# Kernel optimization log

Hardware: AMD Instinct MI355X
Metric: run time of the kernel (lower is better)

The kernel has to match this reference:

```python
import jax, jax.numpy as jnp
import numpy as np

NEG = -1e30  # stand-in for -inf that keeps logaddexp grad-safe


def _ctc_neg_log_likelihood(predictions, labels):
    # predictions: [B, T, C] logits; labels: [B, L] int, -1 = padding.
    # tf.nn.ctc_loss(blank_index=-1) => blank class is C-1.
    B, T, C = predictions.shape
    L = labels.shape[1]
    S = 2 * L + 1
    blank = C - 1

    label_len = jnp.sum((labels != -1).astype(jnp.int32), axis=-1)  # [B]
    labels_c = jnp.where(labels < 0, 0, labels).astype(jnp.int32)

    # Extended label sequence: blank, l1, blank, l2, ..., blank  -> [B, S]
    ext = jnp.full((B, S), blank, dtype=jnp.int32)
    ext = ext.at[:, 1::2].set(labels_c)

    # s-2 transition allowed only at label positions (odd s) with ext[s] != ext[s-2]
    same = jnp.concatenate([jnp.zeros((B, 2), bool), ext[:, 2:] == ext[:, :-2]], axis=1)
    is_label_pos = (jnp.arange(S) % 2 == 1)[None, :]
    allow2 = is_label_pos & ~same  # [B, S]

    # valid extended positions per example: s < 2*label_len + 1
    valid = jnp.arange(S)[None, :] < (2 * label_len + 1)[:, None]  # [B, S]

    log_probs = jax.nn.log_softmax(predictions, axis=-1)  # [B, T, C]
    # emission log-prob for each extended-label slot: [B, T, S]
    lp_ext = jnp.take_along_axis(log_probs, jnp.broadcast_to(ext[:, None, :], (B, T, S)), axis=2)

    has_lab = label_len > 0
    alpha0 = jnp.full((B, S), NEG, dtype=log_probs.dtype)
    alpha0 = alpha0.at[:, 0].set(lp_ext[:, 0, 0])
    alpha0 = alpha0.at[:, 1].set(jnp.where(has_lab, lp_ext[:, 0, 1], NEG))
    alpha0 = jnp.where(valid, alpha0, NEG)

    def step(alpha, lp_t):
        a1 = alpha
        a2 = jnp.pad(alpha, ((0, 0), (1, 0)), constant_values=NEG)[:, :S]
        a3 = jnp.pad(alpha, ((0, 0), (2, 0)), constant_values=NEG)[:, :S]
        a3 = jnp.where(allow2, a3, NEG)
        new = jnp.logaddexp(jnp.logaddexp(a1, a2), a3) + lp_t
        new = jnp.where(valid, new, NEG)
        return new, None

    lp_rest = jnp.moveaxis(lp_ext[:, 1:], 1, 0)  # [T-1, B, S]
    alphaT, _ = jax.lax.scan(step, alpha0, lp_rest)

    idx1 = (2 * label_len)[:, None]              # final blank
    idx2 = jnp.maximum(idx1 - 1, 0)              # final label
    a_end1 = jnp.take_along_axis(alphaT, idx1, axis=1)[:, 0]
    a_end2 = jnp.take_along_axis(alphaT, idx2, axis=1)[:, 0]
    a_end2 = jnp.where(has_lab, a_end2, NEG)
    log_lik = jnp.logaddexp(a_end1, a_end2)
    return -log_lik  # [B]


def setup_inputs() -> dict:
    key = jax.random.key(0)
    k1, k2 = jax.random.split(key)
    B, T, C, L = 1024, 384, 96, 48
    labels = jax.random.randint(k1, (B, L), 0, C - 1).astype(jnp.int64)
    predictions = jax.random.normal(k2, (B, T, C), dtype=jnp.float32)
    return {"labels": labels, "predictions": predictions}


def reference(labels, predictions):
    per_example = _ctc_neg_log_likelihood(predictions, labels)
    return jnp.mean(per_example)
```

## Files before the change

kernel.cpp:

```cpp
#include <hip/hip_runtime.h>

#define NEG (-1e30f)

constexpr int Tt = 384;
constexpr int Cc = 96;
constexpr int Ll = 48;
constexpr int Gg = 8;
constexpr int NG = 24;

__device__ __forceinline__ float lae2(float a, float b) {
    float m = fmaxf(a, b);
    return m + __logf(__expf(a - m) + __expf(b - m));
}
__device__ __forceinline__ float lae3(float a, float b, float c) {
    float m = fmaxf(fmaxf(a, b), c);
    return m + __logf(__expf(a - m) + __expf(b - m) + __expf(c - m));
}

template <bool FWD>
__device__ __forceinline__ void half_pass(const float2* __restrict__ rp2, int lane,
                                          int idx_h, int bitsel, bool allow2,
                                          bool valid_e, bool valid_o,
                                          float& st_e, float& st_o) {
    float2 q[Gg];
    float lpbC[Gg], lplC[Gg], lpbN[Gg], lplN[Gg];

    auto loadg = [&](int g) {
#pragma unroll
        for (int j = 0; j < Gg; ++j) {
            int k = g * Gg + j;
            int t = FWD ? k : (Tt - 1 - k);
            q[j] = (lane < 48) ? rp2[(size_t)t * 48 + lane] : make_float2(NEG, NEG);
        }
    };
    auto lp_from_q = [&](float* lpb, float* lpl, int gnext) {
        float s[Gg], gb[Gg], g0[Gg], g1[Gg];
#pragma unroll
        for (int j = 0; j < Gg; ++j)
            s[j] = (lane < 48) ? (__expf(q[j].x) + __expf(q[j].y)) : 0.0f;
#pragma unroll
        for (int j = 0; j < Gg; ++j) {
            gb[j] = __shfl(q[j].y, 47, 64);
            g0[j] = __shfl(q[j].x, idx_h, 64);
            g1[j] = __shfl(q[j].y, idx_h, 64);
        }
        if (gnext < NG) loadg(gnext);
#pragma unroll
        for (int off = 32; off >= 1; off >>= 1) {
#pragma unroll
            for (int j = 0; j < Gg; ++j) s[j] += __shfl_xor(s[j], off, 64);
        }
#pragma unroll
        for (int j = 0; j < Gg; ++j) {
            float lz = __logf(s[j]);
            lpb[j] = gb[j] - lz;
            lpl[j] = (bitsel ? g1[j] : g0[j]) - lz;
        }
    };

    loadg(0);
    lp_from_q(lpbC, lplC, 1);

    for (int g = 0; g < NG; ++g) {
        if (g + 1 < NG) lp_from_q(lpbN, lplN, g + 2);
#pragma unroll
        for (int j = 0; j < Gg; ++j) {
            if (FWD) {
                float ap = __shfl_up(st_o, 1, 64);
                ap = lane ? ap : NEG;
                float ne = lae2(st_e, ap) + lpbC[j];
                float no = lae3(st_o, st_e, allow2 ? ap : NEG) + lplC[j];
                st_e = valid_e ? ne : NEG;
                st_o = valid_o ? no : NEG;
            } else {
                float en = __shfl_down(st_e, 1, 64);
                float on = __shfl_down(st_o, 1, 64);
                float ne = lae2(st_e, st_o) + lpbC[j];
                float no = lae3(st_o, en, allow2 ? on : NEG) + lplC[j];
                st_e = valid_e ? ne : NEG;
                st_o = valid_o ? no : NEG;
            }
        }
        if (g + 1 < NG) {
#pragma unroll
            for (int j = 0; j < Gg; ++j) { lpbC[j] = lpbN[j]; lplC[j] = lplN[j]; }
        }
    }
}

__global__ __launch_bounds__(64) void zero_kernel(float* o) { *o = 0.0f; }

__global__ __launch_bounds__(128) void ctc_fb(const int* __restrict__ labels,
                                              const float* __restrict__ pred,
                                              float* __restrict__ out,
                                              float invB) {
    const int b    = blockIdx.x;
    const int lane = threadIdx.x & 63;
    const int wv   = threadIdx.x >> 6;
    const float2* rp2 = (const float2*)(pred + (size_t)b * Tt * Cc);

    int v = (lane < Ll) ? labels[(size_t)b * Ll + lane] : -1;
    int present = (lane < Ll) && (v != -1);
    int labv = (v < 0) ? 0 : v;
    unsigned long long pm = __ballot(present);
    int len = __popcll(pm);

    bool valid_e = (lane <= len);
    bool valid_o = (lane < len);
    int idx_h  = labv >> 1;
    int bitsel = labv & 1;
    int lab_p = __shfl_up(labv, 1, 64);
    int lab_n = __shfl_down(labv, 1, 64);

    __shared__ float sbe[64], sbo[64];

    float A_e = NEG, A_o = NEG;
    if (wv == 0) {
        bool allow2 = (lane >= 1) && (labv != lab_p);
        float a_e = (lane == 0) ? 0.0f : NEG;
        float a_o = NEG;
        half_pass<true>(rp2, lane, idx_h, bitsel, allow2, valid_e, valid_o, a_e, a_o);
        float ap = __shfl_up(a_o, 1, 64);
        ap = lane ? ap : NEG;
        A_e = lae2(a_e, ap);
        A_o = lae3(a_o, a_e, allow2 ? ap : NEG);
        A_e = valid_e ? A_e : NEG;
        A_o = valid_o ? A_o : NEG;
    } else {
        bool allow2 = (labv != lab_n);
        float b_e = (lane == len) ? 0.0f : NEG;
        float b_o = NEG;
        half_pass<false>(rp2, lane, idx_h, bitsel, allow2, valid_e, valid_o, b_e, b_o);
        sbe[lane] = b_e;
        sbo[lane] = b_o;
    }
    __syncthreads();

    if (wv == 0) {
        float ve = A_e + sbe[lane];
        float vo = A_o + sbo[lane];
        float m = fmaxf(ve, vo);
#pragma unroll
        for (int off = 32; off >= 1; off >>= 1) m = fmaxf(m, __shfl_xor(m, off, 64));
        float ss = __expf(ve - m) + __expf(vo - m);
#pragma unroll
        for (int off = 32; off >= 1; off >>= 1) ss += __shfl_xor(ss, off, 64);
        float ll = m + __logf(ss);
        if (lane == 0) atomicAdd(out, -ll * invB);
    }
}

extern "C" void kernel_launch(void* const* d_in, const int* in_sizes, int n_in,
                              void* d_out, int out_size, void* d_ws, size_t ws_size,
                              hipStream_t stream) {
    const int*   labels = (const int*)d_in[0];
    const float* pred   = (const float*)d_in[1];
    float*       out    = (float*)d_out;

    const int B = in_sizes[0] / Ll;

    hipLaunchKernelGGL(zero_kernel, dim3(1), dim3(64), 0, stream, out);
    hipLaunchKernelGGL(ctc_fb, dim3(B), dim3(128), 0, stream,
                       labels, pred, out, 1.0f / (float)B);
}
```

Baseline: 253.3 us.

## Run CTC forward-backward in scaled linear probability space with DPP lane shifts

Replaces the log-space logaddexp recursion with a linear-space alpha/beta recursion. Probabilities are renormalised once per 8-step group by a power-of-two exponent kept per lane, and neighbour exponent offsets are propagated with DPP. Emissions become exp times reciprocal of the row sum instead of log differences, and the warp reductions and shifts now use DPP intrinsics instead of __shfl. This removes most transcendental ops from the serial critical path. In exchange it adds per-group rescaling logic and a risk of underflow or precision loss in linear space.

```diff
diff --git a/kernel.cpp b/kernel.cpp
--- a/kernel.cpp
+++ b/kernel.cpp
@@ -1,6 +1,4 @@
 #include <hip/hip_runtime.h>
-
-#define NEG (-1e30f)
 
 constexpr int Tt = 384;
 constexpr int Cc = 96;
@@ -8,82 +6,120 @@
 constexpr int Gg = 8;
 constexpr int NG = 24;
 
-__device__ __forceinline__ float lae2(float a, float b) {
-    float m = fmaxf(a, b);
-    return m + __logf(__expf(a - m) + __expf(b - m));
-}
-__device__ __forceinline__ float lae3(float a, float b, float c) {
-    float m = fmaxf(fmaxf(a, b), c);
-    return m + __logf(__expf(a - m) + __expf(b - m) + __expf(c - m));
+#define L2E 1.4426950408889634f
+#define LN2 0.6931471805599453f
+#define LNEG (-3.0e38f)
+
+template <int CTRL, int RM = 0xF>
+__device__ __forceinline__ float dppf(float x) {
+    return __int_as_float(
+        __builtin_amdgcn_update_dpp(0, __float_as_int(x), CTRL, RM, 0xF, true));
+}
+template <int CTRL>
+__device__ __forceinline__ int dppi(int x) {
+    return __builtin_amdgcn_update_dpp(0, x, CTRL, 0xF, 0xF, true);
+}
+__device__ __forceinline__ float bcast63(float x) {
+    return __int_as_float(__builtin_amdgcn_readlane(__float_as_int(x), 63));
+}
+__device__ __forceinline__ float wsum(float x) {
+    x += dppf<0x111>(x);
+    x += dppf<0x112>(x);
+    x += dppf<0x114>(x);
+    x += dppf<0x118>(x);
+    x += dppf<0x142, 0xA>(x);
+    x += dppf<0x143, 0xC>(x);
+    return bcast63(x);
+}
+__device__ __forceinline__ float shup1(float x) { return dppf<0x138>(x); }
+__device__ __forceinline__ float shdn1(float x) { return dppf<0x130>(x); }
+__device__ __forceinline__ float exp2i(int d) {
+    d = d < -126 ? -126 : (d > 126 ? 126 : d);
+    return __int_as_float((d + 127) << 23);
 }
 
 template <bool FWD>
 __device__ __forceinline__ void half_pass(const float2* __restrict__ rp2, int lane,
-                                          int idx_h, int bitsel, bool allow2,
-                                          bool valid_e, bool valid_o,
-                                          float& st_e, float& st_o) {
+                                          int idx_h, int bitsel, float allow2f,
+                                          float& st_e, float& st_o, int& ls) {
     float2 q[Gg];
-    float lpbC[Gg], lplC[Gg], lpbN[Gg], lplN[Gg];
+    float pbC[Gg], plC[Gg], pbN[Gg], plN[Gg];
 
     auto loadg = [&](int g) {
 #pragma unroll
         for (int j = 0; j < Gg; ++j) {
             int k = g * Gg + j;
             int t = FWD ? k : (Tt - 1 - k);
-            q[j] = (lane < 48) ? rp2[(size_t)t * 48 + lane] : make_float2(NEG, NEG);
+            q[j] = (lane < 48) ? rp2[(size_t)t * 48 + lane] : make_float2(-1e4f, -1e4f);
         }
     };
-    auto lp_from_q = [&](float* lpb, float* lpl, int gnext) {
-        float s[Gg], gb[Gg], g0[Gg], g1[Gg];
-#pragma unroll
-        for (int j = 0; j < Gg; ++j)
-            s[j] = (lane < 48) ? (__expf(q[j].x) + __expf(q[j].y)) : 0.0f;
-#pragma unroll
-        for (int j = 0; j < Gg; ++j) {
-            gb[j] = __shfl(q[j].y, 47, 64);
-            g0[j] = __shfl(q[j].x, idx_h, 64);
-            g1[j] = __shfl(q[j].y, idx_h, 64);
+    auto emit = [&](float* pb, float* pl, int gnext) {
+        float ex[Gg], ey[Gg], s[Gg], gb[Gg], g0[Gg], g1[Gg];
+#pragma unroll
+        for (int j = 0; j < Gg; ++j) {
+            ex[j] = exp2f(q[j].x * L2E);
+            ey[j] = exp2f(q[j].y * L2E);
+            s[j]  = ex[j] + ey[j];
+        }
+#pragma unroll
+        for (int j = 0; j < Gg; ++j) {
+            gb[j] = __shfl(ey[j], 47, 64);
+            g0[j] = __shfl(ex[j], idx_h, 64);
+            g1[j] = __shfl(ey[j], idx_h, 64);
         }
         if (gnext < NG) loadg(gnext);
 #pragma unroll
-        for (int off = 32; off >= 1; off >>= 1) {
-#pragma unroll
-            for (int j = 0; j < Gg; ++j) s[j] += __shfl_xor(s[j], off, 64);
-        }
-#pragma unroll
-        for (int j = 0; j < Gg; ++j) {
-            float lz = __logf(s[j]);
-            lpb[j] = gb[j] - lz;
-            lpl[j] = (bitsel ? g1[j] : g0[j]) - lz;
+        for (int j = 0; j < Gg; ++j) s[j] = wsum(s[j]);
+#pragma unroll
+        for (int j = 0; j < Gg; ++j) {
+            float rZ = __builtin_amdgcn_rcpf(s[j]);
+            pb[j] = gb[j] * rZ;
+            pl[j] = (bitsel ? g1[j] : g0[j]) * rZ;
         }
     };
 
+    float f   = 1.0f;
+    float a2f = allow2f;
+
     loadg(0);
-    lp_from_q(lpbC, lplC, 1);
+    emit(pbC, plC, 1);
 
     for (int g = 0; g < NG; ++g) {
-        if (g + 1 < NG) lp_from_q(lpbN, lplN, g + 2);
+        if (g + 1 < NG) emit(pbN, plN, g + 2);
 #pragma unroll
         for (int j = 0; j < Gg; ++j) {
             if (FWD) {
-                float ap = __shfl_up(st_o, 1, 64);
-                ap = lane ? ap : NEG;
-                float ne = lae2(st_e, ap) + lpbC[j];
-                float no = lae3(st_o, st_e, allow2 ? ap : NEG) + lplC[j];
-                st_e = valid_e ? ne : NEG;
-                st_o = valid_o ? no : NEG;
+                float sh = shup1(st_o);
+                float t0 = st_e + st_o;
+                float ne = fmaf(f, sh, st_e) * pbC[j];
+                float no = fmaf(a2f, sh, t0) * plC[j];
+                st_e = ne; st_o = no;
             } else {
-                float en = __shfl_down(st_e, 1, 64);
-                float on = __shfl_down(st_o, 1, 64);
-                float ne = lae2(st_e, st_o) + lpbC[j];
-                float no = lae3(st_o, en, allow2 ? on : NEG) + lplC[j];
-                st_e = valid_e ? ne : NEG;
-                st_o = valid_o ? no : NEG;
+                float en = shdn1(st_e);
+                float on = shdn1(st_o);
+                float ne = (st_e + st_o) * pbC[j];
+                float no = fmaf(a2f, on, fmaf(f, en, st_o)) * plC[j];
+                st_e = ne; st_o = no;
             }
         }
+        float m = fmaxf(st_e, st_o);
+        bool z = (m == 0.0f);
+        int eb = (__float_as_int(m) >> 23) & 0xFF;
+        eb = eb > 253 ? 253 : eb;
+        float r = z ? 1.0f : __int_as_float((254 - eb) << 23);
+        st_e *= r; st_o *= r;
+        ls += z ? 0 : (eb - 127);
+#pragma unroll
+        for (int it = 0; it < 8; ++it) {
+            int lsn = FWD ? dppi<0x138>(ls) : dppi<0x130>(ls);
+            ls = z ? lsn : ls;
+        }
+        int lsn2 = FWD ? dppi<0x138>(ls) : dppi<0x130>(ls);
+        f = exp2i(lsn2 - ls);
+        a2f = allow2f * f;
         if (g + 1 < NG) {
 #pragma unroll
-            for (int j = 0; j < Gg; ++j) { lpbC[j] = lpbN[j]; lplC[j] = lplN[j]; }
+            for (int j = 0; j < Gg; ++j) { pbC[j] = pbN[j]; plC[j] = plN[j]; }
         }
     }
 }
@@ -105,48 +141,53 @@
     unsigned long long pm = __ballot(present);
     int len = __popcll(pm);
 
-    bool valid_e = (lane <= len);
-    bool valid_o = (lane < len);
     int idx_h  = labv >> 1;
     int bitsel = labv & 1;
-    int lab_p = __shfl_up(labv, 1, 64);
-    int lab_n = __shfl_down(labv, 1, 64);
+    int lab_p = __shfl(labv, (lane - 1) & 63, 64);
+    int lab_n = __shfl(labv, (lane + 1) & 63, 64);
 
     __shared__ float sbe[64], sbo[64];
-
-    float A_e = NEG, A_o = NEG;
+    __shared__ int   slsb[64];
+
+    float Ae = 0.0f, Ao = 0.0f;
+    int ls_f = 0;
     if (wv == 0) {
-        bool allow2 = (lane >= 1) && (labv != lab_p);
-        float a_e = (lane == 0) ? 0.0f : NEG;
-        float a_o = NEG;
-        half_pass<true>(rp2, lane, idx_h, bitsel, allow2, valid_e, valid_o, a_e, a_o);
-        float ap = __shfl_up(a_o, 1, 64);
-        ap = lane ? ap : NEG;
-        A_e = lae2(a_e, ap);
-        A_o = lae3(a_o, a_e, allow2 ? ap : NEG);
-        A_e = valid_e ? A_e : NEG;
-        A_o = valid_o ? A_o : NEG;
+        float allow2f = (lane >= 1 && labv != lab_p) ? 1.0f : 0.0f;
+        float a_e = (lane == 0) ? 1.0f : 0.0f;
+        float a_o = 0.0f;
+        half_pass<true>(rp2, lane, idx_h, bitsel, allow2f, a_e, a_o, ls_f);
+        float sh  = shup1(a_o);
+        int   lsu = dppi<0x138>(ls_f);
+        float fup = exp2i(lsu - ls_f);
+        Ae = fmaf(fup, sh, a_e);
+        Ao = fmaf(allow2f * fup, sh, a_e + a_o);
     } else {
-        bool allow2 = (labv != lab_n);
-        float b_e = (lane == len) ? 0.0f : NEG;
-        float b_o = NEG;
-        half_pass<false>(rp2, lane, idx_h, bitsel, allow2, valid_e, valid_o, b_e, b_o);
-        sbe[lane] = b_e;
-        sbo[lane] = b_o;
+        float allow2f = (labv != lab_n) ? 1.0f : 0.0f;
+        float b_e = (lane == len) ? 1.0f : 0.0f;
+        float b_o = 0.0f;
+        int ls_b = 0;
+        half_pass<false>(rp2, lane, idx_h, bitsel, allow2f, b_e, b_o, ls_b);
+        sbe[lane]  = b_e;
+        sbo[lane]  = b_o;
+        slsb[lane] = ls_b;
     }
     __syncthreads();
 
     if (wv == 0) {
-        float ve = A_e + sbe[lane];
-        float vo = A_o + sbo[lane];
-        float m = fmaxf(ve, vo);
-#pragma unroll
-        for (int off = 32; off >= 1; off >>= 1) m = fmaxf(m, __shfl_xor(m, off, 64));
-        float ss = __expf(ve - m) + __expf(vo - m);
+        float be = sbe[lane], bo = sbo[lane];
+        float base = (float)(ls_f + slsb[lane]);
+        float l1 = (Ae > 0.0f && be > 0.0f) ? __log2f(Ae) + __log2f(be) + base : LNEG;
+        float l2 = (Ao > 0.0f && bo > 0.0f) ? __log2f(Ao) + __log2f(bo) + base : LNEG;
+        float mm = fmaxf(l1, l2);
+#pragma unroll
+        for (int off = 32; off >= 1; off >>= 1) mm = fmaxf(mm, __shfl_xor(mm, off, 64));
+        float ss = exp2f(l1 - mm) + exp2f(l2 - mm);
 #pragma unroll
         for (int off = 32; off >= 1; off >>= 1) ss += __shfl_xor(ss, off, 64);
-        float ll = m + __logf(ss);
-        if (lane == 0) atomicAdd(out, -ll * invB);
+        if (lane == 0) {
+            float ll = (mm + __log2f(ss)) * LN2;
+            atomicAdd(out, -ll * invB);
+        }
     }
 }
 
```

Result: faster. 227.2 us (-10.3%).
